# Optimization experiments

Measured on AMD Instinct MI355X. Metric: run time of the kernel, lower is better.

Reference implementation:

```python
import jax, jax.numpy as jnp
import numpy as np

# Math note: torch does fold(unfold(low_fea,k,pad) * repeat_c(unfold(kernel,1))).
# Because the unfolded low_fea entry at patch (i,j), offset (a,b) is low_fea[c, i-pad+a, j-pad+b],
# fold's overlap-add collapses to: out[n,c,y,x] = low_fea[n,c,y,x] * S[n,y,x], where
#   S[n,y,x] = sum_{a,b in [0,k)} kernel[n, a*k+b, y+pad-a, x+pad-b]  (zero outside bounds).
# We compute S with a zero-padded shifted sum (k*k small static loop) instead of
# materializing the k2*c*h*w unfolded tensor.


def setup_inputs() -> dict:
    key = jax.random.key(0)
    k1, k2 = jax.random.split(key)
    N, K2, C, H, W = 8, 25, 256, 128, 128
    kernel = jax.random.normal(k1, (N, K2, H, W), dtype=jnp.float32)
    low_fea = jax.random.normal(k2, (N, C, H, W), dtype=jnp.float32)
    return {"kernel": kernel, "low_fea": low_fea}


def reference(kernel, low_fea):
    n, c, h, w = low_fea.shape
    k2 = kernel.shape[1]
    k = int(np.sqrt(k2))
    pad = k // 2  # k odd => 2*pad = k-1
    # zero-pad kernel spatially so out-of-bounds taps contribute 0
    Kp = jnp.pad(kernel, ((0, 0), (0, 0), (pad, pad), (pad, pad)))
    # S[n,y,x] = sum_{a,b} kernel[n, a*k+b, y+pad-a, x+pad-b]
    S = jnp.zeros((n, h, w), dtype=low_fea.dtype)
    for a in range(k):
        for b in range(k):
            S = S + Kp[:, a * k + b,
                       2 * pad - a: 2 * pad - a + h,
                       2 * pad - b: 2 * pad - b + w]
    return low_fea * S[:, None, :, :]
```

## Files before the change

kernel.cpp:

```cpp
#include <hip/hip_runtime.h>

#define NN 8
#define CC 256
#define HH 128
#define WW 128
#define KK 5
#define PAD 2

typedef float f4 __attribute__((ext_vector_type(4)));

__global__ __launch_bounds__(128) void s_compute_kernel(
    const float* __restrict__ kern, float* __restrict__ S)
{
    const int blk = blockIdx.x;
    const int n   = blk >> 7;
    const int y   = blk & (HH - 1);
    const int x   = threadIdx.x;

    float s = 0.0f;
    const float* kb = kern + (size_t)n * (KK * KK) * HH * WW;
#pragma unroll
    for (int a = 0; a < KK; ++a) {
        const int yy = y + PAD - a;
        if (yy >= 0 && yy < HH) {
#pragma unroll
            for (int b = 0; b < KK; ++b) {
                const int xx = x + PAD - b;
                if (xx >= 0 && xx < WW) {
                    s += kb[((size_t)(a * KK + b) * HH + yy) * WW + xx];
                }
            }
        }
    }
    S[(size_t)blk * WW + x] = s;
}

#define SCALE_BLOCKS  2048
#define SCALE_THREADS 256
#define SCALE_STRIDE  (SCALE_BLOCKS * SCALE_THREADS)
#define SCALE_ITERS   16

__global__ __launch_bounds__(SCALE_THREADS) void scale_kernel(
    const float* __restrict__ low,
    const float* __restrict__ S,
    float* __restrict__ out)
{
    const int t = blockIdx.x * SCALE_THREADS + threadIdx.x;
    const f4* __restrict__ lf4  = (const f4*)low;
    const f4* __restrict__ S4   = (const f4*)S;
    f4*       __restrict__ out4 = (f4*)out;

#pragma unroll
    for (int it = 0; it < SCALE_ITERS; ++it) {
        const int i    = t + it * SCALE_STRIDE;
        const int xq   = i & 31;
        const int y    = (i >> 5) & (HH - 1);
        const int n    = i >> 20;
        const int sidx = ((((n << 7) | y) << 5) | xq);

        f4 v = __builtin_nontemporal_load(lf4 + i);
        f4 s = S4[sidx];
        f4 r = v * s;
        __builtin_nontemporal_store(r, out4 + i);
    }
}

__global__ __launch_bounds__(256) void fused_scale_kernel(
    const float* __restrict__ kern,
    const float* __restrict__ low,
    float* __restrict__ out)
{
    __shared__ __align__(16) float S[WW];
    const int blk = blockIdx.x;
    const int n   = blk >> 7;
    const int y   = blk & (HH - 1);
    const int tid = threadIdx.x;

    if (tid < WW) {
        const int x = tid;
        float s = 0.0f;
        const float* kb = kern + (size_t)n * (KK * KK) * HH * WW;
#pragma unroll
        for (int a = 0; a < KK; ++a) {
            const int yy = y + PAD - a;
            if (yy >= 0 && yy < HH) {
#pragma unroll
                for (int b = 0; b < KK; ++b) {
                    const int xx = x + PAD - b;
                    if (xx >= 0 && xx < WW) {
                        s += kb[((size_t)(a * KK + b) * HH + yy) * WW + xx];
                    }
                }
            }
        }
        S[x] = s;
    }
    __syncthreads();

    const f4* lf4  = (const f4*)low;
    f4*       out4 = (f4*)out;
    const size_t base4 = (((size_t)n * CC * HH + (size_t)y) * WW) >> 2;
    const int    xq    = tid & 31;
    const f4 s4 = *(const f4*)&S[xq * 4];

#pragma unroll 8
    for (int it = 0; it < 32; ++it) {
        const int    c   = it * 8 + (tid >> 5);
        const size_t idx = base4 + (size_t)c * (HH * WW / 4) + (size_t)xq;
        f4 v = lf4[idx];
        out4[idx] = v * s4;
    }
}

extern "C" void kernel_launch(void* const* d_in, const int* in_sizes, int n_in,
                              void* d_out, int out_size, void* d_ws, size_t ws_size,
                              hipStream_t stream) {
    const float* kern = (const float*)d_in[0];
    const float* low  = (const float*)d_in[1];
    float* out = (float*)d_out;

    const size_t s_bytes = (size_t)NN * HH * WW * sizeof(float);

    if (ws_size >= s_bytes) {
        float* S = (float*)d_ws;
        s_compute_kernel<<<dim3(NN * HH), dim3(128), 0, stream>>>(kern, S);
        scale_kernel<<<dim3(SCALE_BLOCKS), dim3(SCALE_THREADS), 0, stream>>>(low, S, out);
    } else {
        fused_scale_kernel<<<dim3(NN * HH), dim3(256), 0, stream>>>(kern, low, out);
    }
}
```

Baseline: 255.1 us.

## Always use fused single-kernel path with interleaved batch mapping and nontemporal access

Drops the two-kernel path (S computed into workspace, then a separate scale pass) and always launches the fused kernel. Each block computes its row of S in shared memory and then scales all channels of that row. Block-to-(n,y) mapping now interleaves batch in the low bits, and low_fea loads and output stores are nontemporal. This removes one launch and the S round trip through global memory. In exchange, each block recomputes its 25-tap sum before streaming, which may add latency per block.

```diff
diff --git a/kernel.cpp b/kernel.cpp
--- a/kernel.cpp
+++ b/kernel.cpp
@@ -9,77 +9,21 @@
 
 typedef float f4 __attribute__((ext_vector_type(4)));
 
-__global__ __launch_bounds__(128) void s_compute_kernel(
-    const float* __restrict__ kern, float* __restrict__ S)
-{
-    const int blk = blockIdx.x;
-    const int n   = blk >> 7;
-    const int y   = blk & (HH - 1);
-    const int x   = threadIdx.x;
-
-    float s = 0.0f;
-    const float* kb = kern + (size_t)n * (KK * KK) * HH * WW;
-#pragma unroll
-    for (int a = 0; a < KK; ++a) {
-        const int yy = y + PAD - a;
-        if (yy >= 0 && yy < HH) {
-#pragma unroll
-            for (int b = 0; b < KK; ++b) {
-                const int xx = x + PAD - b;
-                if (xx >= 0 && xx < WW) {
-                    s += kb[((size_t)(a * KK + b) * HH + yy) * WW + xx];
-                }
-            }
-        }
-    }
-    S[(size_t)blk * WW + x] = s;
-}
-
-#define SCALE_BLOCKS  2048
-#define SCALE_THREADS 256
-#define SCALE_STRIDE  (SCALE_BLOCKS * SCALE_THREADS)
-#define SCALE_ITERS   16
-
-__global__ __launch_bounds__(SCALE_THREADS) void scale_kernel(
-    const float* __restrict__ low,
-    const float* __restrict__ S,
-    float* __restrict__ out)
-{
-    const int t = blockIdx.x * SCALE_THREADS + threadIdx.x;
-    const f4* __restrict__ lf4  = (const f4*)low;
-    const f4* __restrict__ S4   = (const f4*)S;
-    f4*       __restrict__ out4 = (f4*)out;
-
-#pragma unroll
-    for (int it = 0; it < SCALE_ITERS; ++it) {
-        const int i    = t + it * SCALE_STRIDE;
-        const int xq   = i & 31;
-        const int y    = (i >> 5) & (HH - 1);
-        const int n    = i >> 20;
-        const int sidx = ((((n << 7) | y) << 5) | xq);
-
-        f4 v = __builtin_nontemporal_load(lf4 + i);
-        f4 s = S4[sidx];
-        f4 r = v * s;
-        __builtin_nontemporal_store(r, out4 + i);
-    }
-}
-
-__global__ __launch_bounds__(256) void fused_scale_kernel(
+__global__ __launch_bounds__(256) void fused_kernel(
     const float* __restrict__ kern,
     const float* __restrict__ low,
     float* __restrict__ out)
 {
     __shared__ __align__(16) float S[WW];
-    const int blk = blockIdx.x;
-    const int n   = blk >> 7;
-    const int y   = blk & (HH - 1);
+
+    const int n   = blockIdx.x & (NN - 1);
+    const int y   = blockIdx.x >> 3;
     const int tid = threadIdx.x;
 
     if (tid < WW) {
         const int x = tid;
         float s = 0.0f;
-        const float* kb = kern + (size_t)n * (KK * KK) * HH * WW;
+        const float* kb = kern + (size_t)n * (KK * KK * HH * WW);
 #pragma unroll
         for (int a = 0; a < KK; ++a) {
             const int yy = y + PAD - a;
@@ -88,7 +32,7 @@
                 for (int b = 0; b < KK; ++b) {
                     const int xx = x + PAD - b;
                     if (xx >= 0 && xx < WW) {
-                        s += kb[((size_t)(a * KK + b) * HH + yy) * WW + xx];
+                        s += kb[((a * KK + b) * HH + yy) * WW + xx];
                     }
                 }
             }
@@ -97,18 +41,19 @@
     }
     __syncthreads();
 
-    const f4* lf4  = (const f4*)low;
-    f4*       out4 = (f4*)out;
-    const size_t base4 = (((size_t)n * CC * HH + (size_t)y) * WW) >> 2;
-    const int    xq    = tid & 31;
+    const int xq = tid & 31;
+    const int c0 = tid >> 5;
     const f4 s4 = *(const f4*)&S[xq * 4];
+
+    const f4* __restrict__ lf4 = (const f4*)(low + ((size_t)n * CC * HH + y) * WW);
+    f4* __restrict__       o4  = (f4*)      (out + ((size_t)n * CC * HH + y) * WW);
 
 #pragma unroll 8
     for (int it = 0; it < 32; ++it) {
-        const int    c   = it * 8 + (tid >> 5);
-        const size_t idx = base4 + (size_t)c * (HH * WW / 4) + (size_t)xq;
-        f4 v = lf4[idx];
-        out4[idx] = v * s4;
+        const int    c   = c0 + it * 8;
+        const size_t idx = (size_t)c * (HH * WW / 4) + xq;
+        f4 v = __builtin_nontemporal_load(lf4 + idx);
+        __builtin_nontemporal_store(v * s4, o4 + idx);
     }
 }
 
@@ -118,14 +63,7 @@
     const float* kern = (const float*)d_in[0];
     const float* low  = (const float*)d_in[1];
     float* out = (float*)d_out;
+    (void)d_ws; (void)ws_size;
 
-    const size_t s_bytes = (size_t)NN * HH * WW * sizeof(float);
-
-    if (ws_size >= s_bytes) {
-        float* S = (float*)d_ws;
-        s_compute_kernel<<<dim3(NN * HH), dim3(128), 0, stream>>>(kern, S);
-        scale_kernel<<<dim3(SCALE_BLOCKS), dim3(SCALE_THREADS), 0, stream>>>(low, S, out);
-    } else {
-        fused_scale_kernel<<<dim3(NN * HH), dim3(256), 0, stream>>>(kern, low, out);
-    }
+    fused_kernel<<<dim3(NN * HH), dim3(256), 0, stream>>>(kern, low, out);
 }
```

Result: faster. 247.3 us (-3.1%).
